# Kernel tuning notes

Measured on AMD Instinct MI355X. Metric: run time of the kernel, lower is better.

## Reference

```python
import jax, jax.numpy as jnp
import numpy as np

N, H, E, C, V, K = 4096, 256, 128, 32, 64, 20


def setup_inputs() -> dict:
    key = jax.random.key(0)
    ks = jax.random.split(key, 16)
    f = lambda k, s: jax.random.normal(k, s, dtype=jnp.float32)
    return {
        "vec": f(ks[0], (N, H)),
        "inp": f(ks[1], (N, E)),
        "h_prev": f(ks[2], (N, H)),
        "c_prev": f(ks[3], (N, H)),
        "Wlin": f(ks[4], (C, V, H)) * 0.05,
        "blin": f(ks[5], (C, V)) * 0.05,
        "Wec": f(ks[6], (2, H)) * 0.05,
        "bec": f(ks[7], (2,)) * 0.05,
        "Wrel": f(ks[8], (5, H)) * 0.05,
        "brel": f(ks[9], (5,)) * 0.05,
        "W_ih": f(ks[10], (K, 4 * H, E)) * 0.05,
        "b_ih": f(ks[11], (K, 4 * H)) * 0.05,
        "W_hh": f(ks[12], (K, 4 * H, H)) * 0.05,
        "b_hh": f(ks[13], (K, 4 * H)) * 0.05,
        "category": jax.random.randint(ks[14], (N,), 0, C, dtype=jnp.int32),
        "cell_id": jax.random.randint(ks[15], (N,), 0, K, dtype=jnp.int32),
        "true_idx": jax.random.randint(jax.random.fold_in(key, 100), (N,), 0, V, dtype=jnp.int32),
        "ec_idx": jax.random.randint(jax.random.fold_in(key, 101), (N,), 0, 2, dtype=jnp.int32),
        "rel_idx": jax.random.randint(jax.random.fold_in(key, 102), (N,), 0, 5, dtype=jnp.int32),
    }


def _ce(logits, targets):
    # per-row cross entropy (same math as nn.CrossEntropyLoss per example)
    logp = jax.nn.log_softmax(logits, axis=-1)
    return -jnp.take_along_axis(logp, targets[:, None], axis=-1)[:, 0]


def reference(vec, inp, h_prev, c_prev, Wlin, blin, Wec, bec, Wrel, brel,
              W_ih, b_ih, W_hh, b_hh, category, cell_id, true_idx, ec_idx, rel_idx):
    # --- get_log_odds: per-category tiny linear head, selected by category ---
    logits_all = jnp.einsum('nh,cvh->ncv', vec, Wlin) + blin          # [N,C,V]
    logits = jnp.take_along_axis(logits_all, category[:, None, None].astype(jnp.int32), axis=1)[:, 0]  # [N,V]
    logits_ec = vec @ Wec.T + bec                                      # [N,2]
    logits_rel = vec @ Wrel.T + brel                                   # [N,5]

    # --- calculate_loss: CE over valid children + ec + rel ---
    losses = _ce(logits, true_idx) + _ce(logits_ec, ec_idx) + _ce(logits_rel, rel_idx)  # [N]

    # --- get_next: per-child-index LSTMCell, selected by cell_id ---
    gates_all = (jnp.einsum('ne,kge->nkg', inp, W_ih)
                 + jnp.einsum('nh,kgh->nkg', h_prev, W_hh)
                 + b_ih + b_hh)                                        # [N,K,4H]
    gates = jnp.take_along_axis(gates_all, cell_id[:, None, None].astype(jnp.int32), axis=1)[:, 0]  # [N,4H]
    i, f, g, o = jnp.split(gates, 4, axis=-1)                          # torch LSTMCell gate order i,f,g,o
    c_next = jax.nn.sigmoid(f) * c_prev + jax.nn.sigmoid(i) * jnp.tanh(g)
    h_next = jax.nn.sigmoid(o) * jnp.tanh(c_next)

    # pack: [N, 1 + 2H] = loss | h_next | c_next
    return jnp.concatenate([losses[:, None], h_next, c_next], axis=-1)
```

## Files before the change

kernel.cpp:

```cpp
#include <hip/hip_runtime.h>
#include <hip/hip_bf16.h>
#include <math.h>

#define Nn 4096
#define Hdim 256
#define Edim 128
#define Cdim 32
#define Vdim 64
#define Kdim 20
#define G4H 1024
#define OUTS 513

#define SK 512
#define SC 256
#define RK_OFF 64
#define RC_OFF (RK_OFF + Kdim * SK)

#define OFF_WF 81920
#define WF_BYTES (Kdim * 4 * 12 * 16 * 64 * 8 * 2)
#define OFF_XF (OFF_WF + WF_BYTES)
#define XF_BYTES (Kdim * 8 * 12 * 4 * 64 * 8 * 2)
#define OFF_LF (OFF_XF + XF_BYTES)
#define LF_BYTES (Cdim * 8 * 5 * 64 * 8 * 2)
#define OFF_VF (OFF_LF + LF_BYTES)
#define VF_BYTES (Cdim * 8 * 8 * 2 * 64 * 8 * 2)

#define NWF (Kdim * 4 * 12)
#define NXF (Kdim * 8)
#define NLF (Cdim * 8)
#define NVF (Cdim * 8)
#define FRAG_GRID (NWF + NXF + NLF + NVF)

#define LSTM_BLOCKS (Kdim * 8 * 4)
#define LOSS_BLOCKS (Cdim * 8)
#define MAIN_GRID (LSTM_BLOCKS + LOSS_BLOCKS)

typedef short bf16x8 __attribute__((ext_vector_type(8)));
typedef float f32x4 __attribute__((ext_vector_type(4)));
typedef unsigned short u16;

__device__ __forceinline__ float sigmoidf_(float x) { return 1.0f / (1.0f + expf(-x)); }

__device__ __forceinline__ bf16x8 cvt8(float4 f0, float4 f1) {
    bf16x8 r;
    __hip_bfloat16 h;
    h = __float2bfloat16(f0.x); r[0] = *(short*)&h;
    h = __float2bfloat16(f0.y); r[1] = *(short*)&h;
    h = __float2bfloat16(f0.z); r[2] = *(short*)&h;
    h = __float2bfloat16(f0.w); r[3] = *(short*)&h;
    h = __float2bfloat16(f1.x); r[4] = *(short*)&h;
    h = __float2bfloat16(f1.y); r[5] = *(short*)&h;
    h = __float2bfloat16(f1.z); r[6] = *(short*)&h;
    h = __float2bfloat16(f1.w); r[7] = *(short*)&h;
    return r;
}

__global__ __launch_bounds__(1024) void k_bucket(const int* __restrict__ cell_id,
                                                 const int* __restrict__ category,
                                                 int* __restrict__ ws) {
    __shared__ int cnt[32];
    int t = threadIdx.x;
    if (t < 32) cnt[t] = 0;
    __syncthreads();
    int i0 = t * 4;
    if (blockIdx.x == 0) {
        int4 v = ((const int4*)cell_id)[t];
        int r;
        r = atomicAdd(&cnt[v.x], 1); if (r < SK) ws[RK_OFF + v.x * SK + r] = i0 + 0;
        r = atomicAdd(&cnt[v.y], 1); if (r < SK) ws[RK_OFF + v.y * SK + r] = i0 + 1;
        r = atomicAdd(&cnt[v.z], 1); if (r < SK) ws[RK_OFF + v.z * SK + r] = i0 + 2;
        r = atomicAdd(&cnt[v.w], 1); if (r < SK) ws[RK_OFF + v.w * SK + r] = i0 + 3;
        __syncthreads();
        if (t < 32) ws[t] = min(cnt[t], SK);
    } else {
        int4 v = ((const int4*)category)[t];
        int r;
        r = atomicAdd(&cnt[v.x], 1); if (r < SC) ws[RC_OFF + v.x * SC + r] = i0 + 0;
        r = atomicAdd(&cnt[v.y], 1); if (r < SC) ws[RC_OFF + v.y * SC + r] = i0 + 1;
        r = atomicAdd(&cnt[v.z], 1); if (r < SC) ws[RC_OFF + v.z * SC + r] = i0 + 2;
        r = atomicAdd(&cnt[v.w], 1); if (r < SC) ws[RC_OFF + v.w * SC + r] = i0 + 3;
        __syncthreads();
        if (t < 32) ws[32 + t] = min(cnt[t], SC);
    }
}

__global__ __launch_bounds__(256) void k_frag(
    const float* __restrict__ W_ih, const float* __restrict__ W_hh,
    const float* __restrict__ Wlin, const float* __restrict__ Wec, const float* __restrict__ Wrel,
    const float* __restrict__ inp, const float* __restrict__ h_prev, const float* __restrict__ vec,
    int* __restrict__ ws)
{
    u16* WF = (u16*)((char*)ws + OFF_WF);
    u16* XF = (u16*)((char*)ws + OFF_XF);
    u16* LF = (u16*)((char*)ws + OFF_LF);
    u16* VF = (u16*)((char*)ws + OFF_VF);
    int b = blockIdx.x, t = threadIdx.x;
    int l = t & 63, sub = t >> 6;
    int c16 = l & 15, qd = l >> 4;

    if (b < NWF) {
        int k = b / 48; int r = b - k * 48; int hq = r / 12; int st = r - hq * 12;
        int kk = st * 32 + qd * 8;
        #pragma unroll
        for (int rep = 0; rep < 4; rep++) {
            int idx = sub * 4 + rep;
            int g = idx >> 2, wv = idx & 3;
            int row = g * Hdim + hq * 64 + wv * 16 + c16;
            const float* p = (st < 4)
                ? (W_ih + ((size_t)k * G4H + row) * Edim + kk)
                : (W_hh + ((size_t)k * G4H + row) * Hdim + (kk - Edim));
            float4 lo = *(const float4*)p;
            float4 hi = *(const float4*)(p + 4);
            *(bf16x8*)(WF + ((size_t)(((k * 4 + hq) * 12 + st) * 16 + idx) * 64 + l) * 8) = cvt8(lo, hi);
        }
    } else if (b < NWF + NXF) {
        int b2 = b - NWF; int k = b2 >> 3; int s = b2 & 7;
        int cntk = ws[k];
        int rc = min(64, cntk - s * 64);
        if (rc <= 0) return;
        int m = sub;
        int j = m * 16 + c16;
        int jj = min(j, rc - 1);
        int orig = ws[RK_OFF + k * SK + s * 64 + jj];
        #pragma unroll
        for (int st = 0; st < 12; st++) {
            int kk = st * 32 + qd * 8;
            const float* p = (st < 4) ? inp + (size_t)orig * Edim + kk
                                      : h_prev + (size_t)orig * Hdim + (kk - Edim);
            float4 lo = *(const float4*)p;
            float4 hi = *(const float4*)(p + 4);
            *(bf16x8*)(XF + ((size_t)(((k * 8 + s) * 12 + st) * 4 + m) * 64 + l) * 8) = cvt8(lo, hi);
        }
    } else if (b < NWF + NXF + NLF) {
        int b3 = b - NWF - NXF; int c = b3 >> 3; int st = b3 & 7;
        int kk = st * 32 + qd * 8;
        for (int wg = sub; wg < 5; wg += 4) {
            int lr = wg * 16 + c16;
            bf16x8 v;
            if (lr < 71) {
                const float* p;
                if (lr < 64)      p = Wlin + ((size_t)c * Vdim + lr) * Hdim + kk;
                else if (lr < 66) p = Wec + (size_t)(lr - 64) * Hdim + kk;
                else              p = Wrel + (size_t)(lr - 66) * Hdim + kk;
                float4 lo = *(const float4*)p;
                float4 hi = *(const float4*)(p + 4);
                v = cvt8(lo, hi);
            } else {
                v = (bf16x8){0, 0, 0, 0, 0, 0, 0, 0};
            }
            *(bf16x8*)(LF + ((size_t)((c * 8 + st) * 5 + wg) * 64 + l) * 8) = v;
        }
    } else {
        int b4 = b - NWF - NXF - NLF; int c = b4 >> 3; int s = b4 & 7;
        int cntc = ws[32 + c];
        int rc = min(32, cntc - s * 32);
        if (rc <= 0) return;
        int m = sub & 1, sh = sub >> 1;
        int j = m * 16 + c16;
        int jj = min(j, rc - 1);
        int orig = ws[RC_OFF + c * SC + s * 32 + jj];
        #pragma unroll
        for (int q = 0; q < 4; q++) {
            int st = sh * 4 + q;
            int kk = st * 32 + qd * 8;
            const float* p = vec + (size_t)orig * Hdim + kk;
            float4 lo = *(const float4*)p;
            float4 hi = *(const float4*)(p + 4);
            *(bf16x8*)(VF + ((size_t)(((c * 8 + s) * 8 + st) * 2 + m) * 64 + l) * 8) = cvt8(lo, hi);
        }
    }
}

__global__ __launch_bounds__(256, 3) void k_main(
    const float* __restrict__ c_prev,
    const float* __restrict__ blin, const float* __restrict__ bec, const float* __restrict__ brel,
    const float* __restrict__ b_ih, const float* __restrict__ b_hh,
    const int* __restrict__ true_idx, const int* __restrict__ ec_idx, const int* __restrict__ rel_idx,
    const int* __restrict__ ws,
    float* __restrict__ out)
{
    const u16* WF = (const u16*)((const char*)ws + OFF_WF);
    const u16* XF = (const u16*)((const char*)ws + OFF_XF);
    const u16* LF = (const u16*)((const char*)ws + OFF_LF);
    const u16* VF = (const u16*)((const char*)ws + OFF_VF);

    int b = blockIdx.x, t = threadIdx.x;
    int wv = t >> 6, l = t & 63;
    int l15 = l & 15, quad = l >> 4;
    __shared__ float Lg[32 * 84];

    if (b < LSTM_BLOCKS) {
        int k = b >> 5; int s = (b >> 2) & 7; int hq = b & 3;
        int cntk = ws[k];
        int rcount = min(64, cntk - s * 64);
        if (rcount <= 0) return;

        const u16* xf = XF + (size_t)((k * 8 + s) * 12) * 2048 + (size_t)l * 8;
        const u16* wf = WF + (size_t)((k * 4 + hq) * 12) * 8192 + (size_t)(wv * 512) + (size_t)l * 8;

        f32x4 acc[4][4];
        #pragma unroll
        for (int m = 0; m < 4; m++)
            #pragma unroll
            for (int g = 0; g < 4; g++)
                acc[m][g] = (f32x4){0.f, 0.f, 0.f, 0.f};

        for (int st = 0; st < 12; st++) {
            const u16* xs = xf + st * 2048;
            const u16* wp = wf + st * 8192;
            bf16x8 af[4], bfr[4];
            #pragma unroll
            for (int m = 0; m < 4; m++) af[m] = *(const bf16x8*)(xs + m * 512);
            #pragma unroll
            for (int g = 0; g < 4; g++) bfr[g] = *(const bf16x8*)(wp + g * 2048);
            #pragma unroll
            for (int m = 0; m < 4; m++)
                #pragma unroll
                for (int g = 0; g < 4; g++)
                    acc[m][g] = __builtin_amdgcn_mfma_f32_16x16x32_bf16(af[m], bfr[g], acc[m][g], 0, 0, 0);
        }

        int h = hq * 64 + wv * 16 + l15;
        float bs[4];
        #pragma unroll
        for (int g = 0; g < 4; g++)
            bs[g] = b_ih[(size_t)k * G4H + g * Hdim + h] + b_hh[(size_t)k * G4H + g * Hdim + h];

        int reg_row = ws[RK_OFF + k * SK + s * 64 + min(l, rcount - 1)];

        #pragma unroll
        for (int m = 0; m < 4; m++) {
            #pragma unroll
            for (int reg = 0; reg < 4; reg++) {
                int r = m * 16 + quad * 4 + reg;
                int row = __shfl(reg_row, r);
                if (r < rcount) {
                    float iv = acc[m][0][reg] + bs[0];
                    float fv = acc[m][1][reg] + bs[1];
                    float gv = acc[m][2][reg] + bs[2];
                    float ov = acc[m][3][reg] + bs[3];
                    float cp = c_prev[(size_t)row * Hdim + h];
                    float cn = sigmoidf_(fv) * cp + sigmoidf_(iv) * tanhf(gv);
                    float hn = sigmoidf_(ov) * tanhf(cn);
                    out[(size_t)row * OUTS + 1 + h] = hn;
                    out[(size_t)row * OUTS + 1 + Hdim + h] = cn;
                }
            }
        }
    } else {
        int b2 = b - LSTM_BLOCKS; int c = b2 >> 3; int s = b2 & 7;
        int cntc = ws[32 + c];
        int rcount = min(32, cntc - s * 32);
        if (rcount <= 0) return;

        const u16* vf = VF + (size_t)((c * 8 + s) * 8) * 1024 + (size_t)l * 8;
        const u16* lf = LF + (size_t)(c * 8) * 2560 + (size_t)l * 8;

        f32x4 a0[2], a1[2];
        #pragma unroll
        for (int m = 0; m < 2; m++) { a0[m] = (f32x4){0.f,0.f,0.f,0.f}; a1[m] = (f32x4){0.f,0.f,0.f,0.f}; }

        for (int st = 0; st < 8; st++) {
            bf16x8 af0 = *(const bf16x8*)(vf + st * 1024);
            bf16x8 af1 = *(const bf16x8*)(vf + st * 1024 + 512);
            bf16x8 b0 = *(const bf16x8*)(lf + st * 2560 + wv * 512);
            a0[0] = __builtin_amdgcn_mfma_f32_16x16x32_bf16(af0, b0, a0[0], 0, 0, 0);
            a0[1] = __builtin_amdgcn_mfma_f32_16x16x32_bf16(af1, b0, a0[1], 0, 0, 0);
            if (wv == 3) {
                bf16x8 b1 = *(const bf16x8*)(lf + st * 2560 + 4 * 512);
                a1[0] = __builtin_amdgcn_mfma_f32_16x16x32_bf16(af0, b1, a1[0], 0, 0, 0);
                a1[1] = __builtin_amdgcn_mfma_f32_16x16x32_bf16(af1, b1, a1[1], 0, 0, 0);
            }
        }

        int reg_row = ws[RC_OFF + c * SC + s * 32 + min(l & 31, rcount - 1)];

        {
            int col = wv * 16 + l15;
            float bb = blin[c * Vdim + col];
            #pragma unroll
            for (int m = 0; m < 2; m++)
                #pragma unroll
                for (int reg = 0; reg < 4; reg++)
                    Lg[(m * 16 + quad * 4 + reg) * 84 + col] = a0[m][reg] + bb;
            if (wv == 3) {
                int col1 = 64 + l15;
                float bb1 = (l15 < 2) ? bec[l15] : ((l15 < 7) ? brel[l15 - 2] : 0.f);
                #pragma unroll
                for (int m = 0; m < 2; m++)
                    #pragma unroll
                    for (int reg = 0; reg < 4; reg++)
                        Lg[(m * 16 + quad * 4 + reg) * 84 + col1] = a1[m][reg] + bb1;
            }
        }
        __syncthreads();
        for (int rr = 0; rr < 8; rr++) {
            int r = wv * 8 + rr;
            if (r >= rcount) break;
            int orig = __shfl(reg_row, r);
            float lg = Lg[r * 84 + l];
            float mx = lg;
            for (int ss = 32; ss >= 1; ss >>= 1) mx = fmaxf(mx, __shfl_xor(mx, ss));
            float sm = expf(lg - mx);
            for (int ss = 32; ss >= 1; ss >>= 1) sm += __shfl_xor(sm, ss);
            float lt = __shfl(lg, true_idx[orig]);
            float loss = mx + logf(sm) - lt;
            if (l == 0) {
                float l0 = Lg[r * 84 + 64], l1 = Lg[r * 84 + 65];
                float me2 = fmaxf(l0, l1);
                loss += me2 + logf(expf(l0 - me2) + expf(l1 - me2)) - ((ec_idx[orig] == 0) ? l0 : l1);
                float rl[5] = { Lg[r * 84 + 66], Lg[r * 84 + 67], Lg[r * 84 + 68], Lg[r * 84 + 69], Lg[r * 84 + 70] };
                float mr = rl[0];
                #pragma unroll
                for (int i = 1; i < 5; i++) mr = fmaxf(mr, rl[i]);
                float sr = 0.f;
                #pragma unroll
                for (int i = 0; i < 5; i++) sr += expf(rl[i] - mr);
                loss += mr + logf(sr) - rl[rel_idx[orig]];
                out[(size_t)orig * OUTS] = loss;
            }
        }
    }
}

extern "C" void kernel_launch(void* const* d_in, const int* in_sizes, int n_in,
                              void* d_out, int out_size, void* d_ws, size_t ws_size,
                              hipStream_t stream) {
    const float* vec      = (const float*)d_in[0];
    const float* inp      = (const float*)d_in[1];
    const float* h_prev   = (const float*)d_in[2];
    const float* c_prev   = (const float*)d_in[3];
    const float* Wlin     = (const float*)d_in[4];
    const float* blin     = (const float*)d_in[5];
    const float* Wec      = (const float*)d_in[6];
    const float* bec      = (const float*)d_in[7];
    const float* Wrel     = (const float*)d_in[8];
    const float* brel     = (const float*)d_in[9];
    const float* W_ih     = (const float*)d_in[10];
    const float* b_ih     = (const float*)d_in[11];
    const float* W_hh     = (const float*)d_in[12];
    const float* b_hh     = (const float*)d_in[13];
    const int*   category = (const int*)d_in[14];
    const int*   cell_id  = (const int*)d_in[15];
    const int*   true_idx = (const int*)d_in[16];
    const int*   ec_idx   = (const int*)d_in[17];
    const int*   rel_idx  = (const int*)d_in[18];
    float* out = (float*)d_out;
    int* ws = (int*)d_ws;

    k_bucket<<<2, 1024, 0, stream>>>(cell_id, category, ws);
    k_frag<<<FRAG_GRID, 256, 0, stream>>>(W_ih, W_hh, Wlin, Wec, Wrel, inp, h_prev, vec, ws);
    k_main<<<MAIN_GRID, 256, 0, stream>>>(c_prev, blin, bec, brel, b_ih, b_hh,
                                          true_idx, ec_idx, rel_idx, ws, out);
}
```

Measured before the change: 157.0 us.

## Fuse bf16 fragment packing into main kernel with register-prefetched fp32 loads

Removes the separate k_frag kernel that converted weights and gathered activations into bf16 MFMA fragment layout in the workspace. k_main now loads fp32 weights and gathered rows directly from global memory, converts them to bf16 in registers, and prefetches the next K-step's operands while issuing MFMAs on the current one. This drops one kernel launch and the round-trip write and read of the staged fragments. In exchange, the fp32 weights are re-read and re-converted by every block that shares them, reads are no longer in a pre-swizzled layout, and occupancy drops from 3 to 2 blocks per CU for the added registers.

```diff
diff --git a/kernel.cpp b/kernel.cpp
--- a/kernel.cpp
+++ b/kernel.cpp
@@ -16,28 +16,12 @@
 #define RK_OFF 64
 #define RC_OFF (RK_OFF + Kdim * SK)
 
-#define OFF_WF 81920
-#define WF_BYTES (Kdim * 4 * 12 * 16 * 64 * 8 * 2)
-#define OFF_XF (OFF_WF + WF_BYTES)
-#define XF_BYTES (Kdim * 8 * 12 * 4 * 64 * 8 * 2)
-#define OFF_LF (OFF_XF + XF_BYTES)
-#define LF_BYTES (Cdim * 8 * 5 * 64 * 8 * 2)
-#define OFF_VF (OFF_LF + LF_BYTES)
-#define VF_BYTES (Cdim * 8 * 8 * 2 * 64 * 8 * 2)
-
-#define NWF (Kdim * 4 * 12)
-#define NXF (Kdim * 8)
-#define NLF (Cdim * 8)
-#define NVF (Cdim * 8)
-#define FRAG_GRID (NWF + NXF + NLF + NVF)
-
 #define LSTM_BLOCKS (Kdim * 8 * 4)
 #define LOSS_BLOCKS (Cdim * 8)
 #define MAIN_GRID (LSTM_BLOCKS + LOSS_BLOCKS)
 
 typedef short bf16x8 __attribute__((ext_vector_type(8)));
 typedef float f32x4 __attribute__((ext_vector_type(4)));
-typedef unsigned short u16;
 
 __device__ __forceinline__ float sigmoidf_(float x) { return 1.0f / (1.0f + expf(-x)); }
 
@@ -84,106 +68,18 @@
     }
 }
 
-__global__ __launch_bounds__(256) void k_frag(
-    const float* __restrict__ W_ih, const float* __restrict__ W_hh,
-    const float* __restrict__ Wlin, const float* __restrict__ Wec, const float* __restrict__ Wrel,
-    const float* __restrict__ inp, const float* __restrict__ h_prev, const float* __restrict__ vec,
-    int* __restrict__ ws)
-{
-    u16* WF = (u16*)((char*)ws + OFF_WF);
-    u16* XF = (u16*)((char*)ws + OFF_XF);
-    u16* LF = (u16*)((char*)ws + OFF_LF);
-    u16* VF = (u16*)((char*)ws + OFF_VF);
-    int b = blockIdx.x, t = threadIdx.x;
-    int l = t & 63, sub = t >> 6;
-    int c16 = l & 15, qd = l >> 4;
-
-    if (b < NWF) {
-        int k = b / 48; int r = b - k * 48; int hq = r / 12; int st = r - hq * 12;
-        int kk = st * 32 + qd * 8;
-        #pragma unroll
-        for (int rep = 0; rep < 4; rep++) {
-            int idx = sub * 4 + rep;
-            int g = idx >> 2, wv = idx & 3;
-            int row = g * Hdim + hq * 64 + wv * 16 + c16;
-            const float* p = (st < 4)
-                ? (W_ih + ((size_t)k * G4H + row) * Edim + kk)
-                : (W_hh + ((size_t)k * G4H + row) * Hdim + (kk - Edim));
-            float4 lo = *(const float4*)p;
-            float4 hi = *(const float4*)(p + 4);
-            *(bf16x8*)(WF + ((size_t)(((k * 4 + hq) * 12 + st) * 16 + idx) * 64 + l) * 8) = cvt8(lo, hi);
-        }
-    } else if (b < NWF + NXF) {
-        int b2 = b - NWF; int k = b2 >> 3; int s = b2 & 7;
-        int cntk = ws[k];
-        int rc = min(64, cntk - s * 64);
-        if (rc <= 0) return;
-        int m = sub;
-        int j = m * 16 + c16;
-        int jj = min(j, rc - 1);
-        int orig = ws[RK_OFF + k * SK + s * 64 + jj];
-        #pragma unroll
-        for (int st = 0; st < 12; st++) {
-            int kk = st * 32 + qd * 8;
-            const float* p = (st < 4) ? inp + (size_t)orig * Edim + kk
-                                      : h_prev + (size_t)orig * Hdim + (kk - Edim);
-            float4 lo = *(const float4*)p;
-            float4 hi = *(const float4*)(p + 4);
-            *(bf16x8*)(XF + ((size_t)(((k * 8 + s) * 12 + st) * 4 + m) * 64 + l) * 8) = cvt8(lo, hi);
-        }
-    } else if (b < NWF + NXF + NLF) {
-        int b3 = b - NWF - NXF; int c = b3 >> 3; int st = b3 & 7;
-        int kk = st * 32 + qd * 8;
-        for (int wg = sub; wg < 5; wg += 4) {
-            int lr = wg * 16 + c16;
-            bf16x8 v;
-            if (lr < 71) {
-                const float* p;
-                if (lr < 64)      p = Wlin + ((size_t)c * Vdim + lr) * Hdim + kk;
-                else if (lr < 66) p = Wec + (size_t)(lr - 64) * Hdim + kk;
-                else              p = Wrel + (size_t)(lr - 66) * Hdim + kk;
-                float4 lo = *(const float4*)p;
-                float4 hi = *(const float4*)(p + 4);
-                v = cvt8(lo, hi);
-            } else {
-                v = (bf16x8){0, 0, 0, 0, 0, 0, 0, 0};
-            }
-            *(bf16x8*)(LF + ((size_t)((c * 8 + st) * 5 + wg) * 64 + l) * 8) = v;
-        }
-    } else {
-        int b4 = b - NWF - NXF - NLF; int c = b4 >> 3; int s = b4 & 7;
-        int cntc = ws[32 + c];
-        int rc = min(32, cntc - s * 32);
-        if (rc <= 0) return;
-        int m = sub & 1, sh = sub >> 1;
-        int j = m * 16 + c16;
-        int jj = min(j, rc - 1);
-        int orig = ws[RC_OFF + c * SC + s * 32 + jj];
-        #pragma unroll
-        for (int q = 0; q < 4; q++) {
-            int st = sh * 4 + q;
-            int kk = st * 32 + qd * 8;
-            const float* p = vec + (size_t)orig * Hdim + kk;
-            float4 lo = *(const float4*)p;
-            float4 hi = *(const float4*)(p + 4);
-            *(bf16x8*)(VF + ((size_t)(((c * 8 + s) * 8 + st) * 2 + m) * 64 + l) * 8) = cvt8(lo, hi);
-        }
-    }
-}
-
-__global__ __launch_bounds__(256, 3) void k_main(
-    const float* __restrict__ c_prev,
-    const float* __restrict__ blin, const float* __restrict__ bec, const float* __restrict__ brel,
-    const float* __restrict__ b_ih, const float* __restrict__ b_hh,
+__global__ __launch_bounds__(256, 2) void k_main(
+    const float* __restrict__ vec, const float* __restrict__ inp,
+    const float* __restrict__ h_prev, const float* __restrict__ c_prev,
+    const float* __restrict__ Wlin, const float* __restrict__ blin,
+    const float* __restrict__ Wec, const float* __restrict__ bec,
+    const float* __restrict__ Wrel, const float* __restrict__ brel,
+    const float* __restrict__ W_ih, const float* __restrict__ b_ih,
+    const float* __restrict__ W_hh, const float* __restrict__ b_hh,
     const int* __restrict__ true_idx, const int* __restrict__ ec_idx, const int* __restrict__ rel_idx,
     const int* __restrict__ ws,
     float* __restrict__ out)
 {
-    const u16* WF = (const u16*)((const char*)ws + OFF_WF);
-    const u16* XF = (const u16*)((const char*)ws + OFF_XF);
-    const u16* LF = (const u16*)((const char*)ws + OFF_LF);
-    const u16* VF = (const u16*)((const char*)ws + OFF_VF);
-
     int b = blockIdx.x, t = threadIdx.x;
     int wv = t >> 6, l = t & 63;
     int l15 = l & 15, quad = l >> 4;
@@ -195,8 +91,28 @@
         int rcount = min(64, cntk - s * 64);
         if (rcount <= 0) return;
 
-        const u16* xf = XF + (size_t)((k * 8 + s) * 12) * 2048 + (size_t)l * 8;
-        const u16* wf = WF + (size_t)((k * 4 + hq) * 12) * 8192 + (size_t)(wv * 512) + (size_t)l * 8;
+        int reg_row = ws[RK_OFF + k * SK + s * 64 + min(l, rcount - 1)];
+
+        const float* xbi[4]; const float* xbh[4];
+        #pragma unroll
+        for (int m = 0; m < 4; m++) {
+            int xr = __shfl(reg_row, m * 16 + l15);
+            xbi[m] = inp    + (size_t)xr * Edim + quad * 8;
+            xbh[m] = h_prev + (size_t)xr * Hdim + quad * 8;
+        }
+        int wrow = hq * 64 + wv * 16 + l15;
+        const float* wbi[4]; const float* wbh[4];
+        #pragma unroll
+        for (int g = 0; g < 4; g++) {
+            wbi[g] = W_ih + ((size_t)k * G4H + g * Hdim + wrow) * Edim + quad * 8;
+            wbh[g] = W_hh + ((size_t)k * G4H + g * Hdim + wrow) * Hdim + quad * 8;
+        }
+
+        int h = hq * 64 + wv * 16 + l15;
+        float bs[4];
+        #pragma unroll
+        for (int g = 0; g < 4; g++)
+            bs[g] = b_ih[(size_t)k * G4H + g * Hdim + h] + b_hh[(size_t)k * G4H + g * Hdim + h];
 
         f32x4 acc[4][4];
         #pragma unroll
@@ -205,28 +121,46 @@
             for (int g = 0; g < 4; g++)
                 acc[m][g] = (f32x4){0.f, 0.f, 0.f, 0.f};
 
+        float4 fx[4][2], fw[4][2];
+        #pragma unroll
+        for (int m = 0; m < 4; m++) {
+            fx[m][0] = *(const float4*)(xbi[m]);
+            fx[m][1] = *(const float4*)(xbi[m] + 4);
+        }
+        #pragma unroll
+        for (int g = 0; g < 4; g++) {
+            fw[g][0] = *(const float4*)(wbi[g]);
+            fw[g][1] = *(const float4*)(wbi[g] + 4);
+        }
+
+        #pragma unroll
         for (int st = 0; st < 12; st++) {
-            const u16* xs = xf + st * 2048;
-            const u16* wp = wf + st * 8192;
             bf16x8 af[4], bfr[4];
             #pragma unroll
-            for (int m = 0; m < 4; m++) af[m] = *(const bf16x8*)(xs + m * 512);
-            #pragma unroll
-            for (int g = 0; g < 4; g++) bfr[g] = *(const bf16x8*)(wp + g * 2048);
+            for (int m = 0; m < 4; m++) af[m] = cvt8(fx[m][0], fx[m][1]);
+            #pragma unroll
+            for (int g = 0; g < 4; g++) bfr[g] = cvt8(fw[g][0], fw[g][1]);
+            if (st < 11) {
+                int s1 = st + 1;
+                #pragma unroll
+                for (int g = 0; g < 4; g++) {
+                    const float* p = (s1 < 4) ? wbi[g] + s1 * 32 : wbh[g] + (s1 - 4) * 32;
+                    fw[g][0] = *(const float4*)p;
+                    fw[g][1] = *(const float4*)(p + 4);
+                }
+                #pragma unroll
+                for (int m = 0; m < 4; m++) {
+                    const float* p = (s1 < 4) ? xbi[m] + s1 * 32 : xbh[m] + (s1 - 4) * 32;
+                    fx[m][0] = *(const float4*)p;
+                    fx[m][1] = *(const float4*)(p + 4);
+                }
+            }
             #pragma unroll
             for (int m = 0; m < 4; m++)
                 #pragma unroll
                 for (int g = 0; g < 4; g++)
                     acc[m][g] = __builtin_amdgcn_mfma_f32_16x16x32_bf16(af[m], bfr[g], acc[m][g], 0, 0, 0);
         }
-
-        int h = hq * 64 + wv * 16 + l15;
-        float bs[4];
-        #pragma unroll
-        for (int g = 0; g < 4; g++)
-            bs[g] = b_ih[(size_t)k * G4H + g * Hdim + h] + b_hh[(size_t)k * G4H + g * Hdim + h];
-
-        int reg_row = ws[RK_OFF + k * SK + s * 64 + min(l, rcount - 1)];
 
         #pragma unroll
         for (int m = 0; m < 4; m++) {
@@ -253,27 +187,60 @@
         int rcount = min(32, cntc - s * 32);
         if (rcount <= 0) return;
 
-        const u16* vf = VF + (size_t)((c * 8 + s) * 8) * 1024 + (size_t)l * 8;
-        const u16* lf = LF + (size_t)(c * 8) * 2560 + (size_t)l * 8;
+        int reg_row = ws[RC_OFF + c * SC + s * 32 + min(l & 31, rcount - 1)];
+
+        const float* vb[2];
+        #pragma unroll
+        for (int m = 0; m < 2; m++) {
+            int xr = __shfl(reg_row, m * 16 + l15);
+            vb[m] = vec + (size_t)xr * Hdim + quad * 8;
+        }
+        const float* wb0 = Wlin + ((size_t)c * Vdim + wv * 16 + l15) * Hdim + quad * 8;
+        const float* wb1 = nullptr;
+        if (wv == 3) {
+            if (l15 < 2)      wb1 = Wec + (size_t)l15 * Hdim + quad * 8;
+            else if (l15 < 7) wb1 = Wrel + (size_t)(l15 - 2) * Hdim + quad * 8;
+        }
 
         f32x4 a0[2], a1[2];
         #pragma unroll
         for (int m = 0; m < 2; m++) { a0[m] = (f32x4){0.f,0.f,0.f,0.f}; a1[m] = (f32x4){0.f,0.f,0.f,0.f}; }
 
+        float4 fv0[2][2], fw0[2], fw1[2];
+        #pragma unroll
+        for (int m = 0; m < 2; m++) {
+            fv0[m][0] = *(const float4*)(vb[m]);
+            fv0[m][1] = *(const float4*)(vb[m] + 4);
+        }
+        fw0[0] = *(const float4*)(wb0);
+        fw0[1] = *(const float4*)(wb0 + 4);
+        if (wb1) { fw1[0] = *(const float4*)(wb1); fw1[1] = *(const float4*)(wb1 + 4); }
+        else     { fw1[0] = (float4){0,0,0,0};     fw1[1] = (float4){0,0,0,0}; }
+
+        #pragma unroll
         for (int st = 0; st < 8; st++) {
-            bf16x8 af0 = *(const bf16x8*)(vf + st * 1024);
-            bf16x8 af1 = *(const bf16x8*)(vf + st * 1024 + 512);
-            bf16x8 b0 = *(const bf16x8*)(lf + st * 2560 + wv * 512);
+            bf16x8 af0 = cvt8(fv0[0][0], fv0[0][1]);
+            bf16x8 af1 = cvt8(fv0[1][0], fv0[1][1]);
+            bf16x8 b0 = cvt8(fw0[0], fw0[1]);
+            bf16x8 b1 = cvt8(fw1[0], fw1[1]);
+            if (st < 7) {
+                int o = (st + 1) * 32;
+                #pragma unroll
+                for (int m = 0; m < 2; m++) {
+                    fv0[m][0] = *(const float4*)(vb[m] + o);
+                    fv0[m][1] = *(const float4*)(vb[m] + o + 4);
+                }
+                fw0[0] = *(const float4*)(wb0 + o);
+                fw0[1] = *(const float4*)(wb0 + o + 4);
+                if (wb1) { fw1[0] = *(const float4*)(wb1 + o); fw1[1] = *(const float4*)(wb1 + o + 4); }
+            }
             a0[0] = __builtin_amdgcn_mfma_f32_16x16x32_bf16(af0, b0, a0[0], 0, 0, 0);
             a0[1] = __builtin_amdgcn_mfma_f32_16x16x32_bf16(af1, b0, a0[1], 0, 0, 0);
             if (wv == 3) {
-                bf16x8 b1 = *(const bf16x8*)(lf + st * 2560 + 4 * 512);
                 a1[0] = __builtin_amdgcn_mfma_f32_16x16x32_bf16(af0, b1, a1[0], 0, 0, 0);
                 a1[1] = __builtin_amdgcn_mfma_f32_16x16x32_bf16(af1, b1, a1[1], 0, 0, 0);
             }
         }
-
-        int reg_row = ws[RC_OFF + c * SC + s * 32 + min(l & 31, rcount - 1)];
 
         {
             int col = wv * 16 + l15;
@@ -349,7 +316,7 @@
     int* ws = (int*)d_ws;
 
     k_bucket<<<2, 1024, 0, stream>>>(cell_id, category, ws);
-    k_frag<<<FRAG_GRID, 256, 0, stream>>>(W_ih, W_hh, Wlin, Wec, Wrel, inp, h_prev, vec, ws);
-    k_main<<<MAIN_GRID, 256, 0, stream>>>(c_prev, blin, bec, brel, b_ih, b_hh,
-                                          true_idx, ec_idx, rel_idx, ws, out);
+    k_main<<<MAIN_GRID, 256, 0, stream>>>(
+        vec, inp, h_prev, c_prev, Wlin, blin, Wec, bec, Wrel, brel,
+        W_ih, b_ih, W_hh, b_hh, true_idx, ec_idx, rel_idx, ws, out);
 }
```

Result: slower. 196.6 us (+25.3%).
